# Kernel tuning notes

Hardware: AMD Instinct MI355X
Metric: run time of the kernel (lower is better)

The kernel has to match this reference:

```python
import jax, jax.numpy as jnp
import numpy as np

HEADS = 16

def setup_inputs() -> dict:
    key = jax.random.key(0)
    ks = jax.random.split(key, 5)
    dim = 1024
    x = jax.random.normal(ks[0], (2, 2048, dim), dtype=jnp.float32)
    scale = 1.0 / np.sqrt(dim)
    Wq = jax.random.normal(ks[1], (dim, dim), dtype=jnp.float32) * scale
    Wk = jax.random.normal(ks[2], (dim, dim), dtype=jnp.float32) * scale
    Wv = jax.random.normal(ks[3], (dim, dim), dtype=jnp.float32) * scale
    Wo = jax.random.normal(ks[4], (dim, dim), dtype=jnp.float32) * scale
    return {"x": x, "Wq": Wq, "Wk": Wk, "Wv": Wv, "Wo": Wo}

def reference(x, Wq, Wk, Wv, Wo):
    b, n, dim = x.shape
    h = HEADS
    d = dim // h
    # projections: torch Linear y = x @ W.T (W is [out,in])
    def split_heads(t):
        return t.reshape(b, n, h, d).transpose(0, 2, 1, 3)  # b h n d
    q = split_heads(x @ Wq.T)
    k = split_heads(x @ Wk.T)
    v = split_heads(x @ Wv.T)
    scale = jnp.asarray(d, x.dtype) ** -0.5
    dots = jnp.einsum('bhid,bhjd->bhij', q, k) * scale
    # causal mask: positions j > i masked (triu with diagonal 1 since i == j)
    i_idx = jnp.arange(n)[:, None]
    j_idx = jnp.arange(n)[None, :]
    mask_value = -jnp.finfo(dots.dtype).max
    dots = jnp.where(j_idx > i_idx, mask_value, dots)
    attn = jax.nn.softmax(dots, axis=-1)  # dropout p=0 (eval) is identity
    out = jnp.einsum('bhij,bhjd->bhid', attn, v)
    out = out.transpose(0, 2, 1, 3).reshape(b, n, dim)
    return out @ Wo.T
```

## Files before the change

### kernel.cpp

```cpp
#include <hip/hip_runtime.h>
#include <hip/hip_bf16.h>

#define BATCH 2
#define SEQ   2048
#define DIM   1024
#define HEADS 16
#define DIMH  64
#define BK    32
#define LOG2E 1.44269504088896340736f
#define SM_SHIFT 16.0f

typedef __attribute__((ext_vector_type(8))) short short8;
typedef __attribute__((ext_vector_type(4))) short short4v;
typedef __attribute__((ext_vector_type(4))) float floatx4;

static __device__ __forceinline__ void gload_lds16(const void* g, void* l) {
    __builtin_amdgcn_global_load_lds(
        (const __attribute__((address_space(1))) void*)g,
        (__attribute__((address_space(3))) void*)l, 16, 0, 0);
}

static __device__ __forceinline__ unsigned pk_trunc(float a, float b) {
    return (__float_as_uint(b) & 0xffff0000u) | (__float_as_uint(a) >> 16);
}

__global__ __launch_bounds__(256) void conv_all(
    const float* __restrict__ x,  const float* __restrict__ Wq,
    const float* __restrict__ Wk, const float* __restrict__ Wv,
    const float* __restrict__ Wo,
    __hip_bfloat16* __restrict__ dst, __hip_bfloat16* __restrict__ dwo)
{
    const size_t NX = (size_t)BATCH * SEQ * DIM;
    const size_t NW = (size_t)DIM * DIM;
    size_t i = ((size_t)blockIdx.x * 256 + threadIdx.x) * 4;
    if (i >= NX + 4 * NW) return;
    const float* src; __hip_bfloat16* d;
    if (i < NX) { src = x + i; d = dst + i; }
    else if (i < NX + 3 * NW) {
        size_t j = i - NX;
        int w = (int)(j >> 20);
        src = ((w == 0) ? Wq : (w == 1) ? Wk : Wv) + (j & (NW - 1));
        d = dst + i;
    } else {
        size_t off = i - (NX + 3 * NW);
        src = Wo + off; d = dwo + off;
    }
    floatx4 f = *reinterpret_cast<const floatx4*>(src);
    short4v o;
    #pragma unroll
    for (int e = 0; e < 4; ++e) {
        __hip_bfloat16 t = __float2bfloat16(f[e]);
        o[e] = *reinterpret_cast<short*>(&t);
    }
    *reinterpret_cast<short4v*>(d) = o;
}

__global__ __launch_bounds__(256) void gemm_qkv(
    const __hip_bfloat16* __restrict__ xbf,
    const __hip_bfloat16* __restrict__ wbf,
    __hip_bfloat16* __restrict__ qkv)
{
    __shared__ __align__(16) short As[128 * BK];
    __shared__ __align__(16) short Bs[128 * BK];

    const int tid  = threadIdx.x;
    const int wv   = tid >> 6;
    const int lane = tid & 63;
    const int quad = lane >> 4;
    const int l16  = lane & 15;
    const int wm   = wv >> 1, wn = wv & 1;
    const int m0   = blockIdx.x * 128;
    const int n0   = blockIdx.y * 128;
    const int z    = n0 >> 10;
    __hip_bfloat16* out = qkv + (size_t)z * (BATCH * SEQ * DIM);

    const int srow = tid >> 2;
    const int scol = (tid & 3) * 8;

    floatx4 acc[4][4] = {};

    for (int k0 = 0; k0 < DIM; k0 += BK) {
        __syncthreads();
        #pragma unroll
        for (int i = 0; i < 2; ++i) {
            const __hip_bfloat16* ga = xbf + (size_t)(m0 + srow + i * 64) * DIM + k0 + scol;
            const __hip_bfloat16* gb = wbf + (size_t)(n0 + srow + i * 64) * DIM + k0 + scol;
            gload_lds16(ga, (char*)As + i * 4096 + wv * 1024);
            gload_lds16(gb, (char*)Bs + i * 4096 + wv * 1024);
        }
        __syncthreads();

        short8 af[4], bf[4];
        #pragma unroll
        for (int mt = 0; mt < 4; ++mt)
            af[mt] = *reinterpret_cast<const short8*>(&As[(wm * 64 + mt * 16 + l16) * 32 + quad * 8]);
        #pragma unroll
        for (int nt = 0; nt < 4; ++nt)
            bf[nt] = *reinterpret_cast<const short8*>(&Bs[(wn * 64 + nt * 16 + l16) * 32 + quad * 8]);
        #pragma unroll
        for (int mt = 0; mt < 4; ++mt)
            #pragma unroll
            for (int nt = 0; nt < 4; ++nt)
                acc[mt][nt] = __builtin_amdgcn_mfma_f32_16x16x32_bf16(
                    af[mt], bf[nt], acc[mt][nt], 0, 0, 0);
    }

    const float esc = (z == 0) ? (0.125f * LOG2E) : 1.0f;
    #pragma unroll
    for (int mt = 0; mt < 4; ++mt) {
        #pragma unroll
        for (int nt = 0; nt < 4; ++nt) {
            const int n  = n0 + wn * 64 + nt * 16 + l16;
            const int hh = (n >> 6) & 15, dv = n & 63;
            #pragma unroll
            for (int r = 0; r < 4; ++r) {
                const int m  = m0 + wm * 64 + mt * 16 + quad * 4 + r;
                const int bb = m >> 11, nn = m & (SEQ - 1);
                const float v = acc[mt][nt][r] * esc;
                if (z < 2)
                    out[((size_t)(bb * HEADS + hh) * SEQ + nn) * DIMH + dv] = __float2bfloat16(v);
                else
                    out[((size_t)(bb * HEADS + hh) * DIMH + dv) * SEQ + nn] = __float2bfloat16(v);
            }
        }
    }
}

__global__ __launch_bounds__(256) void gemm_out(
    const __hip_bfloat16* __restrict__ qhs,
    const __hip_bfloat16* __restrict__ W,
    float* __restrict__ C)
{
    __shared__ __align__(16) short As[128 * BK];
    __shared__ __align__(16) short Bs[128 * BK];

    const int tid  = threadIdx.x;
    const int wv   = tid >> 6;
    const int lane = tid & 63;
    const int quad = lane >> 4;
    const int l16  = lane & 15;
    const int wm   = wv >> 1, wn = wv & 1;
    const int m0   = blockIdx.x * 128;
    const int n0   = blockIdx.y * 128;

    const int srow = tid >> 2;
    const int scol = (tid & 3) * 8;

    floatx4 acc[4][4] = {};

    for (int k0 = 0; k0 < DIM; k0 += BK) {
        const int h    = k0 >> 6;
        const int koff = k0 & 63;
        __syncthreads();
        #pragma unroll
        for (int i = 0; i < 2; ++i) {
            const int m  = m0 + srow + i * 64;
            const int bb = m >> 11, nn = m & (SEQ - 1);
            gload_lds16(qhs + ((size_t)(bb * HEADS + h) * SEQ + nn) * DIMH + koff + scol,
                        (char*)As + i * 4096 + wv * 1024);
            gload_lds16(W + (size_t)(n0 + srow + i * 64) * DIM + k0 + scol,
                        (char*)Bs + i * 4096 + wv * 1024);
        }
        __syncthreads();

        short8 af[4], bf[4];
        #pragma unroll
        for (int mt = 0; mt < 4; ++mt)
            af[mt] = *reinterpret_cast<const short8*>(&As[(wm * 64 + mt * 16 + l16) * 32 + quad * 8]);
        #pragma unroll
        for (int nt = 0; nt < 4; ++nt)
            bf[nt] = *reinterpret_cast<const short8*>(&Bs[(wn * 64 + nt * 16 + l16) * 32 + quad * 8]);
        #pragma unroll
        for (int mt = 0; mt < 4; ++mt)
            #pragma unroll
            for (int nt = 0; nt < 4; ++nt)
                acc[mt][nt] = __builtin_amdgcn_mfma_f32_16x16x32_bf16(
                    af[mt], bf[nt], acc[mt][nt], 0, 0, 0);
    }

    #pragma unroll
    for (int mt = 0; mt < 4; ++mt)
        #pragma unroll
        for (int nt = 0; nt < 4; ++nt) {
            const int n = n0 + wn * 64 + nt * 16 + l16;
            #pragma unroll
            for (int r = 0; r < 4; ++r) {
                const int m = m0 + wm * 64 + mt * 16 + quad * 4 + r;
                C[(size_t)m * DIM + n] = acc[mt][nt][r];
            }
        }
}

__global__ __launch_bounds__(256) void attn_causal(
    __hip_bfloat16* __restrict__ qkv)
{
    __shared__ __align__(16) short kt[64 * 64];
    __shared__ __align__(16) short vt[64 * 64];
    __shared__ __align__(16) short pt[2][16 * 72];

    const int id    = blockIdx.x;
    const int combo = id & 31;
    const int p     = id >> 5;
    const int b     = combo >> 4;
    const int h     = combo & 15;
    const int tA = p, tB = 63 - p;
    const int nA = (tA + 2) >> 1;
    const int nB = (tB + 2) >> 1;
    const int total = nA + nB;

    const size_t hoff = (size_t)(b * HEADS + h) * SEQ * DIMH;
    const size_t one  = (size_t)BATCH * SEQ * DIM;
    __hip_bfloat16* qb        = qkv + hoff;
    const __hip_bfloat16* kb  = qkv + one + hoff;
    const __hip_bfloat16* vtg = qkv + 2 * one + hoff;

    const int tid  = threadIdx.x;
    const int wv   = tid >> 6;
    const int g    = wv >> 1;
    const int jh   = wv & 1;
    const int lane = tid & 63;
    const int quad = lane >> 4;
    const int l16  = lane & 15;
    const int xr   = l16 & 7;

    const short8 kone8 = {0x3F80, 0x3F80, 0x3F80, 0x3F80,
                          0x3F80, 0x3F80, 0x3F80, 0x3F80};

    int q16 = tA * 32 + g * 16;
    short8 aq0 = *reinterpret_cast<const short8*>(qb + (size_t)(q16 + l16) * DIMH + quad * 8);
    short8 aq1 = *reinterpret_cast<const short8*>(qb + (size_t)(q16 + l16) * DIMH + 32 + quad * 8);
    floatx4 oacc[4] = {};
    floatx4 lsum = {};

    short8 kreg[2], vreg[2];
    #pragma unroll
    for (int i = 0; i < 2; ++i) {
        const int c = tid + 256 * i;
        const int row = c >> 3, jc = c & 7;
        kreg[i] = *reinterpret_cast<const short8*>(kb + (size_t)row * DIMH + jc * 8);
        vreg[i] = *reinterpret_cast<const short8*>(vtg + (size_t)row * SEQ + jc * 8);
    }

    for (int s = 0; s < total; ++s) {
        const bool lastA = (s == nA - 1);
        const int j0 = ((s < nA) ? s : s - nA) * 64;

        __syncthreads();
        #pragma unroll
        for (int i = 0; i < 2; ++i) {
            const int c = tid + 256 * i;
            const int row = c >> 3, jc = c & 7;
            const int off = row * 64 + ((jc ^ (row & 7)) * 8);
            *reinterpret_cast<short8*>(&kt[off]) = kreg[i];
            *reinterpret_cast<short8*>(&vt[off]) = vreg[i];
        }
        __syncthreads();

        if (s + 1 < total) {
            const int s2 = s + 1;
            const int j1 = ((s2 < nA) ? s2 : s2 - nA) * 64;
            #pragma unroll
            for (int i = 0; i < 2; ++i) {
                const int c = tid + 256 * i;
                const int row = c >> 3, jc = c & 7;
                kreg[i] = *reinterpret_cast<const short8*>(kb + (size_t)(j1 + row) * DIMH + jc * 8);
                vreg[i] = *reinterpret_cast<const short8*>(vtg + (size_t)row * SEQ + j1 + jc * 8);
            }
        }

        floatx4 st[2];
        #pragma unroll
        for (int tt = 0; tt < 2; ++tt) {
            const int t  = jh * 2 + tt;
            const int rw = t * 16 + l16;
            short8 a0 = *reinterpret_cast<const short8*>(&kt[rw * 64 + (quad ^ xr) * 8]);
            short8 a1 = *reinterpret_cast<const short8*>(&kt[rw * 64 + ((quad + 4) ^ xr) * 8]);
            floatx4 zz = {};
            zz     = __builtin_amdgcn_mfma_f32_16x16x32_bf16(a0, aq0, zz, 0, 0, 0);
            st[tt] = __builtin_amdgcn_mfma_f32_16x16x32_bf16(a1, aq1, zz, 0, 0, 0);
        }

        if (j0 + 63 > q16) {
            const int qg = q16 + l16;
            #pragma unroll
            for (int tt = 0; tt < 2; ++tt)
                #pragma unroll
                for (int r = 0; r < 4; ++r) {
                    const int jg = j0 + (jh * 2 + tt) * 16 + quad * 4 + r;
                    if (jg > qg) st[tt][r] = -3.0e38f;
                }
        }

        #pragma unroll
        for (int tt = 0; tt < 2; ++tt)
            #pragma unroll
            for (int r = 0; r < 4; ++r)
                st[tt][r] = __builtin_amdgcn_exp2f(st[tt][r] - SM_SHIFT);

        #pragma unroll
        for (int tt = 0; tt < 2; ++tt) {
            const int t = jh * 2 + tt;
            *reinterpret_cast<unsigned*>(&pt[g][l16 * 72 + t * 16 + quad * 4]) =
                pk_trunc(st[tt][0], st[tt][1]);
            *reinterpret_cast<unsigned*>(&pt[g][l16 * 72 + t * 16 + quad * 4 + 2]) =
                pk_trunc(st[tt][2], st[tt][3]);
        }
        short8 ph = *reinterpret_cast<const short8*>(&pt[g][l16 * 72 + jh * 32 + quad * 8]);

        lsum = __builtin_amdgcn_mfma_f32_16x16x32_bf16(kone8, ph, lsum, 0, 0, 0);

        #pragma unroll
        for (int dt = 0; dt < 4; ++dt) {
            const int rw = dt * 16 + l16;
            short8 vh = *reinterpret_cast<const short8*>(&vt[rw * 64 + ((quad + 4 * jh) ^ xr) * 8]);
            oacc[dt] = __builtin_amdgcn_mfma_f32_16x16x32_bf16(vh, ph, oacc[dt], 0, 0, 0);
        }

        if (lastA || s == total - 1) {
            __syncthreads();
            float* xch = reinterpret_cast<float*>(kt);
            float* xls = reinterpret_cast<float*>(vt);
            if (jh == 1) {
                #pragma unroll
                for (int dt = 0; dt < 4; ++dt)
                    #pragma unroll
                    for (int r = 0; r < 4; ++r)
                        xch[g * 1024 + (dt * 4 + r) * 64 + lane] = oacc[dt][r];
                xls[g * 64 + lane] = lsum[0];
            }
            __syncthreads();
            if (jh == 0) {
                const float rl = 1.0f / (lsum[0] + xls[g * 64 + lane]);
                #pragma unroll
                for (int dt = 0; dt < 4; ++dt)
                    #pragma unroll
                    for (int r = 0; r < 4; ++r) {
                        const float ov = oacc[dt][r] + xch[g * 1024 + (dt * 4 + r) * 64 + lane];
                        qb[(size_t)(q16 + l16) * DIMH + dt * 16 + quad * 4 + r] =
                            __float2bfloat16(ov * rl);
                    }
            }
            if (lastA) {
                q16 = tB * 32 + g * 16;
                aq0 = *reinterpret_cast<const short8*>(qb + (size_t)(q16 + l16) * DIMH + quad * 8);
                aq1 = *reinterpret_cast<const short8*>(qb + (size_t)(q16 + l16) * DIMH + 32 + quad * 8);
                #pragma unroll
                for (int dt = 0; dt < 4; ++dt)
                    #pragma unroll
                    for (int r = 0; r < 4; ++r) oacc[dt][r] = 0.f;
                #pragma unroll
                for (int r = 0; r < 4; ++r) lsum[r] = 0.f;
            }
        }
    }
}


extern "C" void kernel_launch(void* const* d_in, const int* in_sizes, int n_in,
                              void* d_out, int out_size, void* d_ws, size_t ws_size,
                              hipStream_t stream) {
    const float* x  = (const float*)d_in[0];
    const float* Wq = (const float*)d_in[1];
    const float* Wk = (const float*)d_in[2];
    const float* Wv = (const float*)d_in[3];
    const float* Wo = (const float*)d_in[4];

    __hip_bfloat16* qkv  = (__hip_bfloat16*)d_ws;
    __hip_bfloat16* wobf = (__hip_bfloat16*)((char*)d_ws + (size_t)24 * 1024 * 1024);

    __hip_bfloat16* xbf = (__hip_bfloat16*)d_out;
    __hip_bfloat16* wbf = xbf + (size_t)BATCH * SEQ * DIM;

    conv_all  <<<8192, 256, 0, stream>>>(x, Wq, Wk, Wv, Wo, xbf, wobf);
    gemm_qkv  <<<dim3((BATCH * SEQ) / 128, (3 * DIM) / 128), 256, 0, stream>>>(xbf, wbf, qkv);
    attn_causal<<<dim3(1024), 256, 0, stream>>>(qkv);
    gemm_out  <<<dim3((BATCH * SEQ) / 128, DIM / 128), 256, 0, stream>>>(qkv, wobf, (float*)d_out);
}
```

Before: 189.0 us.

## Process two K/V tiles per barrier pair in causal attention

The attention loop now stages two 64-row K/V tiles per iteration into doubled LDS buffers, so each pair of tiles shares one pair of block barriers instead of paying a barrier pair per tile. Register prefetch covers two tiles ahead, and the A/B segments run as separate loops with the output epilogue between them. This cuts synchronisation cost and gives more independent MFMA work between barriers, at the price of twice the LDS and more prefetch registers, which may lower occupancy.

```diff
diff --git a/kernel.cpp b/kernel.cpp
--- a/kernel.cpp
+++ b/kernel.cpp
@@ -194,8 +194,8 @@
 __global__ __launch_bounds__(256) void attn_causal(
     __hip_bfloat16* __restrict__ qkv)
 {
-    __shared__ __align__(16) short kt[64 * 64];
-    __shared__ __align__(16) short vt[64 * 64];
+    __shared__ __align__(16) short kt[2][64 * 64];
+    __shared__ __align__(16) short vt[2][64 * 64];
     __shared__ __align__(16) short pt[2][16 * 72];
 
     const int id    = blockIdx.x;
@@ -206,7 +206,6 @@
     const int tA = p, tB = 63 - p;
     const int nA = (tA + 2) >> 1;
     const int nB = (tB + 2) >> 1;
-    const int total = nA + nB;
 
     const size_t hoff = (size_t)(b * HEADS + h) * SEQ * DIMH;
     const size_t one  = (size_t)BATCH * SEQ * DIM;
@@ -232,127 +231,143 @@
     floatx4 oacc[4] = {};
     floatx4 lsum = {};
 
-    short8 kreg[2], vreg[2];
-    #pragma unroll
-    for (int i = 0; i < 2; ++i) {
-        const int c = tid + 256 * i;
-        const int row = c >> 3, jc = c & 7;
-        kreg[i] = *reinterpret_cast<const short8*>(kb + (size_t)row * DIMH + jc * 8);
-        vreg[i] = *reinterpret_cast<const short8*>(vtg + (size_t)row * SEQ + jc * 8);
-    }
-
-    for (int s = 0; s < total; ++s) {
-        const bool lastA = (s == nA - 1);
-        const int j0 = ((s < nA) ? s : s - nA) * 64;
-
-        __syncthreads();
-        #pragma unroll
-        for (int i = 0; i < 2; ++i) {
-            const int c = tid + 256 * i;
-            const int row = c >> 3, jc = c & 7;
-            const int off = row * 64 + ((jc ^ (row & 7)) * 8);
-            *reinterpret_cast<short8*>(&kt[off]) = kreg[i];
-            *reinterpret_cast<short8*>(&vt[off]) = vreg[i];
-        }
-        __syncthreads();
-
-        if (s + 1 < total) {
-            const int s2 = s + 1;
-            const int j1 = ((s2 < nA) ? s2 : s2 - nA) * 64;
-            #pragma unroll
-            for (int i = 0; i < 2; ++i) {
-                const int c = tid + 256 * i;
-                const int row = c >> 3, jc = c & 7;
-                kreg[i] = *reinterpret_cast<const short8*>(kb + (size_t)(j1 + row) * DIMH + jc * 8);
-                vreg[i] = *reinterpret_cast<const short8*>(vtg + (size_t)row * SEQ + j1 + jc * 8);
+    short8 kreg[4], vreg[4];
+
+#define LOADREG(slot, j0v) do {                                                     \
+    _Pragma("unroll")                                                               \
+    for (int i_ = 0; i_ < 2; ++i_) {                                                \
+        const int cc_ = tid + 256 * i_;                                             \
+        const int row_ = cc_ >> 3, jc_ = cc_ & 7;                                   \
+        kreg[(slot) * 2 + i_] = *reinterpret_cast<const short8*>(                   \
+            kb + (size_t)((j0v) + row_) * DIMH + jc_ * 8);                          \
+        vreg[(slot) * 2 + i_] = *reinterpret_cast<const short8*>(                   \
+            vtg + (size_t)row_ * SEQ + (j0v) + jc_ * 8);                            \
+    } } while (0)
+
+#define COMMIT(slot) do {                                                           \
+    _Pragma("unroll")                                                               \
+    for (int i_ = 0; i_ < 2; ++i_) {                                                \
+        const int cc_ = tid + 256 * i_;                                             \
+        const int row_ = cc_ >> 3, jc_ = cc_ & 7;                                   \
+        const int off_ = row_ * 64 + ((jc_ ^ (row_ & 7)) * 8);                      \
+        *reinterpret_cast<short8*>(&kt[slot][off_]) = kreg[(slot) * 2 + i_];        \
+        *reinterpret_cast<short8*>(&vt[slot][off_]) = vreg[(slot) * 2 + i_];        \
+    } } while (0)
+
+#define COMPUTE(slot, j0v) do {                                                     \
+    const int j0_ = (j0v);                                                          \
+    floatx4 st_[2];                                                                 \
+    _Pragma("unroll")                                                               \
+    for (int tt_ = 0; tt_ < 2; ++tt_) {                                             \
+        const int t_  = jh * 2 + tt_;                                               \
+        const int rw_ = t_ * 16 + l16;                                              \
+        short8 a0_ = *reinterpret_cast<const short8*>(                              \
+            &kt[slot][rw_ * 64 + (quad ^ xr) * 8]);                                 \
+        short8 a1_ = *reinterpret_cast<const short8*>(                              \
+            &kt[slot][rw_ * 64 + ((quad + 4) ^ xr) * 8]);                           \
+        floatx4 zz_ = {};                                                           \
+        zz_     = __builtin_amdgcn_mfma_f32_16x16x32_bf16(a0_, aq0, zz_, 0, 0, 0);  \
+        st_[tt_] = __builtin_amdgcn_mfma_f32_16x16x32_bf16(a1_, aq1, zz_, 0, 0, 0); \
+    }                                                                               \
+    if (j0_ + 63 > q16) {                                                           \
+        const int qg_ = q16 + l16;                                                  \
+        _Pragma("unroll")                                                           \
+        for (int tt_ = 0; tt_ < 2; ++tt_)                                           \
+            _Pragma("unroll")                                                       \
+            for (int r_ = 0; r_ < 4; ++r_) {                                        \
+                const int jg_ = j0_ + (jh * 2 + tt_) * 16 + quad * 4 + r_;          \
+                if (jg_ > qg_) st_[tt_][r_] = -3.0e38f;                             \
+            }                                                                       \
+    }                                                                               \
+    _Pragma("unroll")                                                               \
+    for (int tt_ = 0; tt_ < 2; ++tt_)                                               \
+        _Pragma("unroll")                                                           \
+        for (int r_ = 0; r_ < 4; ++r_)                                              \
+            st_[tt_][r_] = __builtin_amdgcn_exp2f(st_[tt_][r_] - SM_SHIFT);         \
+    _Pragma("unroll")                                                               \
+    for (int tt_ = 0; tt_ < 2; ++tt_) {                                             \
+        const int t_ = jh * 2 + tt_;                                                \
+        *reinterpret_cast<unsigned*>(&pt[g][l16 * 72 + t_ * 16 + quad * 4]) =       \
+            pk_trunc(st_[tt_][0], st_[tt_][1]);                                     \
+        *reinterpret_cast<unsigned*>(&pt[g][l16 * 72 + t_ * 16 + quad * 4 + 2]) =   \
+            pk_trunc(st_[tt_][2], st_[tt_][3]);                                     \
+    }                                                                               \
+    short8 ph_ = *reinterpret_cast<const short8*>(                                  \
+        &pt[g][l16 * 72 + jh * 32 + quad * 8]);                                     \
+    lsum = __builtin_amdgcn_mfma_f32_16x16x32_bf16(kone8, ph_, lsum, 0, 0, 0);      \
+    _Pragma("unroll")                                                               \
+    for (int dt_ = 0; dt_ < 4; ++dt_) {                                             \
+        const int rw_ = dt_ * 16 + l16;                                             \
+        short8 vh_ = *reinterpret_cast<const short8*>(                              \
+            &vt[slot][rw_ * 64 + ((quad + 4 * jh) ^ xr) * 8]);                      \
+        oacc[dt_] = __builtin_amdgcn_mfma_f32_16x16x32_bf16(vh_, ph_, oacc[dt_], 0, 0, 0); \
+    } } while (0)
+
+    LOADREG(0, 0);
+    if (nA >= 2) LOADREG(1, 64);
+
+    for (int seg = 0; seg < 2; ++seg) {
+        const int n = seg ? nB : nA;
+        for (int s = 0; s < n; s += 2) {
+            const int cnt = (n - s >= 2) ? 2 : 1;
+
+            __syncthreads();
+            COMMIT(0);
+            if (cnt == 2) COMMIT(1);
+            __syncthreads();
+
+            int ns = s + 2, nseg = seg;
+            if (ns >= n) { ns = 0; nseg = seg + 1; }
+            if (nseg < 2) {
+                const int nn2  = nseg ? nB : nA;
+                const int ncnt = (nn2 - ns >= 2) ? 2 : 1;
+                LOADREG(0, ns * 64);
+                if (ncnt == 2) LOADREG(1, ns * 64 + 64);
             }
-        }
-
-        floatx4 st[2];
-        #pragma unroll
-        for (int tt = 0; tt < 2; ++tt) {
-            const int t  = jh * 2 + tt;
-            const int rw = t * 16 + l16;
-            short8 a0 = *reinterpret_cast<const short8*>(&kt[rw * 64 + (quad ^ xr) * 8]);
-            short8 a1 = *reinterpret_cast<const short8*>(&kt[rw * 64 + ((quad + 4) ^ xr) * 8]);
-            floatx4 zz = {};
-            zz     = __builtin_amdgcn_mfma_f32_16x16x32_bf16(a0, aq0, zz, 0, 0, 0);
-            st[tt] = __builtin_amdgcn_mfma_f32_16x16x32_bf16(a1, aq1, zz, 0, 0, 0);
-        }
-
-        if (j0 + 63 > q16) {
-            const int qg = q16 + l16;
-            #pragma unroll
-            for (int tt = 0; tt < 2; ++tt)
+
+            COMPUTE(0, s * 64);
+            if (cnt == 2) COMPUTE(1, s * 64 + 64);
+        }
+
+        __syncthreads();
+        float* xch = reinterpret_cast<float*>(kt);
+        float* xls = reinterpret_cast<float*>(vt);
+        if (jh == 1) {
+            #pragma unroll
+            for (int dt = 0; dt < 4; ++dt)
+                #pragma unroll
+                for (int r = 0; r < 4; ++r)
+                    xch[g * 1024 + (dt * 4 + r) * 64 + lane] = oacc[dt][r];
+            xls[g * 64 + lane] = lsum[0];
+        }
+        __syncthreads();
+        if (jh == 0) {
+            const float rl = 1.0f / (lsum[0] + xls[g * 64 + lane]);
+            #pragma unroll
+            for (int dt = 0; dt < 4; ++dt)
                 #pragma unroll
                 for (int r = 0; r < 4; ++r) {
-                    const int jg = j0 + (jh * 2 + tt) * 16 + quad * 4 + r;
-                    if (jg > qg) st[tt][r] = -3.0e38f;
+                    const float ov = oacc[dt][r] + xch[g * 1024 + (dt * 4 + r) * 64 + lane];
+                    qb[(size_t)(q16 + l16) * DIMH + dt * 16 + quad * 4 + r] =
+                        __float2bfloat16(ov * rl);
                 }
         }
-
-        #pragma unroll
-        for (int tt = 0; tt < 2; ++tt)
-            #pragma unroll
-            for (int r = 0; r < 4; ++r)
-                st[tt][r] = __builtin_amdgcn_exp2f(st[tt][r] - SM_SHIFT);
-
-        #pragma unroll
-        for (int tt = 0; tt < 2; ++tt) {
-            const int t = jh * 2 + tt;
-            *reinterpret_cast<unsigned*>(&pt[g][l16 * 72 + t * 16 + quad * 4]) =
-                pk_trunc(st[tt][0], st[tt][1]);
-            *reinterpret_cast<unsigned*>(&pt[g][l16 * 72 + t * 16 + quad * 4 + 2]) =
-                pk_trunc(st[tt][2], st[tt][3]);
-        }
-        short8 ph = *reinterpret_cast<const short8*>(&pt[g][l16 * 72 + jh * 32 + quad * 8]);
-
-        lsum = __builtin_amdgcn_mfma_f32_16x16x32_bf16(kone8, ph, lsum, 0, 0, 0);
-
-        #pragma unroll
-        for (int dt = 0; dt < 4; ++dt) {
-            const int rw = dt * 16 + l16;
-            short8 vh = *reinterpret_cast<const short8*>(&vt[rw * 64 + ((quad + 4 * jh) ^ xr) * 8]);
-            oacc[dt] = __builtin_amdgcn_mfma_f32_16x16x32_bf16(vh, ph, oacc[dt], 0, 0, 0);
-        }
-
-        if (lastA || s == total - 1) {
-            __syncthreads();
-            float* xch = reinterpret_cast<float*>(kt);
-            float* xls = reinterpret_cast<float*>(vt);
-            if (jh == 1) {
+        if (seg == 0) {
+            q16 = tB * 32 + g * 16;
+            aq0 = *reinterpret_cast<const short8*>(qb + (size_t)(q16 + l16) * DIMH + quad * 8);
+            aq1 = *reinterpret_cast<const short8*>(qb + (size_t)(q16 + l16) * DIMH + 32 + quad * 8);
+            #pragma unroll
+            for (int dt = 0; dt < 4; ++dt)
                 #pragma unroll
-                for (int dt = 0; dt < 4; ++dt)
-                    #pragma unroll
-                    for (int r = 0; r < 4; ++r)
-                        xch[g * 1024 + (dt * 4 + r) * 64 + lane] = oacc[dt][r];
-                xls[g * 64 + lane] = lsum[0];
-            }
-            __syncthreads();
-            if (jh == 0) {
-                const float rl = 1.0f / (lsum[0] + xls[g * 64 + lane]);
-                #pragma unroll
-                for (int dt = 0; dt < 4; ++dt)
-                    #pragma unroll
-                    for (int r = 0; r < 4; ++r) {
-                        const float ov = oacc[dt][r] + xch[g * 1024 + (dt * 4 + r) * 64 + lane];
-                        qb[(size_t)(q16 + l16) * DIMH + dt * 16 + quad * 4 + r] =
-                            __float2bfloat16(ov * rl);
-                    }
-            }
-            if (lastA) {
-                q16 = tB * 32 + g * 16;
-                aq0 = *reinterpret_cast<const short8*>(qb + (size_t)(q16 + l16) * DIMH + quad * 8);
-                aq1 = *reinterpret_cast<const short8*>(qb + (size_t)(q16 + l16) * DIMH + 32 + quad * 8);
-                #pragma unroll
-                for (int dt = 0; dt < 4; ++dt)
-                    #pragma unroll
-                    for (int r = 0; r < 4; ++r) oacc[dt][r] = 0.f;
-                #pragma unroll
-                for (int r = 0; r < 4; ++r) lsum[r] = 0.f;
-            }
-        }
-    }
+                for (int r = 0; r < 4; ++r) oacc[dt][r] = 0.f;
+            #pragma unroll
+            for (int r = 0; r < 4; ++r) lsum[r] = 0.f;
+        }
+    }
+
+#undef LOADREG
+#undef COMMIT
+#undef COMPUTE
 }
 
 
```

Result: no change. 189.5 us (+0.3%).

## Load K and V fragments directly from global into registers, drop LDS staging

Applied to the files above, without the earlier changes.

The attention kernel no longer stages K and V tiles through shared memory with two block-wide barriers per step. Each wave now loads its MFMA operand fragments for K and V straight from global memory, double-buffering K in registers and loading V each iteration. This removes the per-step LDS writes, reads and __syncthreads. In exchange, the two waves sharing a query group each fetch their own slices with less coalesced 16-byte accesses, and the V loads are not prefetched, so their latency may be exposed.

```diff
diff --git a/kernel.cpp b/kernel.cpp
--- a/kernel.cpp
+++ b/kernel.cpp
@@ -194,9 +194,9 @@
 __global__ __launch_bounds__(256) void attn_causal(
     __hip_bfloat16* __restrict__ qkv)
 {
-    __shared__ __align__(16) short kt[64 * 64];
-    __shared__ __align__(16) short vt[64 * 64];
     __shared__ __align__(16) short pt[2][16 * 72];
+    __shared__ __align__(16) float xch[2][1024];
+    __shared__ float xls[2][64];
 
     const int id    = blockIdx.x;
     const int combo = id & 31;
@@ -221,7 +221,6 @@
     const int lane = tid & 63;
     const int quad = lane >> 4;
     const int l16  = lane & 15;
-    const int xr   = l16 & 7;
 
     const short8 kone8 = {0x3F80, 0x3F80, 0x3F80, 0x3F80,
                           0x3F80, 0x3F80, 0x3F80, 0x3F80};
@@ -232,52 +231,44 @@
     floatx4 oacc[4] = {};
     floatx4 lsum = {};
 
-    short8 kreg[2], vreg[2];
+    const size_t kbase = (size_t)(jh * 32 + l16) * DIMH + quad * 8;
+    const size_t vbase = (size_t)l16 * SEQ + jh * 32 + quad * 8;
+
+    short8 kc[2][2], kn[2][2];
     #pragma unroll
-    for (int i = 0; i < 2; ++i) {
-        const int c = tid + 256 * i;
-        const int row = c >> 3, jc = c & 7;
-        kreg[i] = *reinterpret_cast<const short8*>(kb + (size_t)row * DIMH + jc * 8);
-        vreg[i] = *reinterpret_cast<const short8*>(vtg + (size_t)row * SEQ + jc * 8);
-    }
+    for (int tt = 0; tt < 2; ++tt)
+        #pragma unroll
+        for (int hf = 0; hf < 2; ++hf)
+            kc[tt][hf] = *reinterpret_cast<const short8*>(
+                kb + kbase + (size_t)tt * 16 * DIMH + hf * 32);
 
     for (int s = 0; s < total; ++s) {
         const bool lastA = (s == nA - 1);
         const int j0 = ((s < nA) ? s : s - nA) * 64;
 
-        __syncthreads();
-        #pragma unroll
-        for (int i = 0; i < 2; ++i) {
-            const int c = tid + 256 * i;
-            const int row = c >> 3, jc = c & 7;
-            const int off = row * 64 + ((jc ^ (row & 7)) * 8);
-            *reinterpret_cast<short8*>(&kt[off]) = kreg[i];
-            *reinterpret_cast<short8*>(&vt[off]) = vreg[i];
-        }
-        __syncthreads();
+        short8 vc[4];
+        #pragma unroll
+        for (int dt = 0; dt < 4; ++dt)
+            vc[dt] = *reinterpret_cast<const short8*>(
+                vtg + vbase + (size_t)dt * 16 * SEQ + j0);
+
+        floatx4 st[2];
+        #pragma unroll
+        for (int tt = 0; tt < 2; ++tt) {
+            floatx4 zz = {};
+            zz     = __builtin_amdgcn_mfma_f32_16x16x32_bf16(kc[tt][0], aq0, zz, 0, 0, 0);
+            st[tt] = __builtin_amdgcn_mfma_f32_16x16x32_bf16(kc[tt][1], aq1, zz, 0, 0, 0);
+        }
 
         if (s + 1 < total) {
             const int s2 = s + 1;
             const int j1 = ((s2 < nA) ? s2 : s2 - nA) * 64;
             #pragma unroll
-            for (int i = 0; i < 2; ++i) {
-                const int c = tid + 256 * i;
-                const int row = c >> 3, jc = c & 7;
-                kreg[i] = *reinterpret_cast<const short8*>(kb + (size_t)(j1 + row) * DIMH + jc * 8);
-                vreg[i] = *reinterpret_cast<const short8*>(vtg + (size_t)row * SEQ + j1 + jc * 8);
-            }
-        }
-
-        floatx4 st[2];
-        #pragma unroll
-        for (int tt = 0; tt < 2; ++tt) {
-            const int t  = jh * 2 + tt;
-            const int rw = t * 16 + l16;
-            short8 a0 = *reinterpret_cast<const short8*>(&kt[rw * 64 + (quad ^ xr) * 8]);
-            short8 a1 = *reinterpret_cast<const short8*>(&kt[rw * 64 + ((quad + 4) ^ xr) * 8]);
-            floatx4 zz = {};
-            zz     = __builtin_amdgcn_mfma_f32_16x16x32_bf16(a0, aq0, zz, 0, 0, 0);
-            st[tt] = __builtin_amdgcn_mfma_f32_16x16x32_bf16(a1, aq1, zz, 0, 0, 0);
+            for (int tt = 0; tt < 2; ++tt)
+                #pragma unroll
+                for (int hf = 0; hf < 2; ++hf)
+                    kn[tt][hf] = *reinterpret_cast<const short8*>(
+                        kb + kbase + (size_t)(j1 + tt * 16) * DIMH + hf * 32);
         }
 
         if (j0 + 63 > q16) {
@@ -310,32 +301,27 @@
         lsum = __builtin_amdgcn_mfma_f32_16x16x32_bf16(kone8, ph, lsum, 0, 0, 0);
 
         #pragma unroll
-        for (int dt = 0; dt < 4; ++dt) {
-            const int rw = dt * 16 + l16;
-            short8 vh = *reinterpret_cast<const short8*>(&vt[rw * 64 + ((quad + 4 * jh) ^ xr) * 8]);
-            oacc[dt] = __builtin_amdgcn_mfma_f32_16x16x32_bf16(vh, ph, oacc[dt], 0, 0, 0);
-        }
+        for (int dt = 0; dt < 4; ++dt)
+            oacc[dt] = __builtin_amdgcn_mfma_f32_16x16x32_bf16(vc[dt], ph, oacc[dt], 0, 0, 0);
 
         if (lastA || s == total - 1) {
             __syncthreads();
-            float* xch = reinterpret_cast<float*>(kt);
-            float* xls = reinterpret_cast<float*>(vt);
             if (jh == 1) {
                 #pragma unroll
                 for (int dt = 0; dt < 4; ++dt)
                     #pragma unroll
                     for (int r = 0; r < 4; ++r)
-                        xch[g * 1024 + (dt * 4 + r) * 64 + lane] = oacc[dt][r];
-                xls[g * 64 + lane] = lsum[0];
+                        xch[g][(dt * 4 + r) * 64 + lane] = oacc[dt][r];
+                xls[g][lane] = lsum[0];
             }
             __syncthreads();
             if (jh == 0) {
-                const float rl = 1.0f / (lsum[0] + xls[g * 64 + lane]);
+                const float rl = 1.0f / (lsum[0] + xls[g][lane]);
                 #pragma unroll
                 for (int dt = 0; dt < 4; ++dt)
                     #pragma unroll
                     for (int r = 0; r < 4; ++r) {
-                        const float ov = oacc[dt][r] + xch[g * 1024 + (dt * 4 + r) * 64 + lane];
+                        const float ov = oacc[dt][r] + xch[g][(dt * 4 + r) * 64 + lane];
                         qb[(size_t)(q16 + l16) * DIMH + dt * 16 + quad * 4 + r] =
                             __float2bfloat16(ov * rl);
                     }
@@ -352,6 +338,12 @@
                 for (int r = 0; r < 4; ++r) lsum[r] = 0.f;
             }
         }
+
+        #pragma unroll
+        for (int tt = 0; tt < 2; ++tt)
+            #pragma unroll
+            for (int hf = 0; hf < 2; ++hf)
+                kc[tt][hf] = kn[tt][hf];
     }
 }
 
```

After: 262.3 us. 1.39x slower.

## Double GEMM K-tile to 64 with XOR-swizzled LDS and raise MFMA wave priority

Applied to the files above, without the earlier changes.

Both projection GEMMs now stage a 64-wide K slice per iteration instead of 32. Each LDS row chunk is XOR-swizzled so the wider rows avoid bank conflicts on the MFMA fragment reads. This halves the number of barrier pairs and load phases per GEMM, at the cost of double the shared memory per block, which can lower occupancy. In the attention kernel, s_setprio brackets the MFMA sections so waves issuing matrix ops get scheduling priority over waves doing softmax work.

```diff
diff --git a/kernel.cpp b/kernel.cpp
--- a/kernel.cpp
+++ b/kernel.cpp
@@ -6,7 +6,7 @@
 #define DIM   1024
 #define HEADS 16
 #define DIMH  64
-#define BK    32
+#define BK    64
 #define LOG2E 1.44269504088896340736f
 #define SM_SHIFT 16.0f
 
@@ -74,35 +74,41 @@
     const int z    = n0 >> 10;
     __hip_bfloat16* out = qkv + (size_t)z * (BATCH * SEQ * DIM);
 
-    const int srow = tid >> 2;
-    const int scol = (tid & 3) * 8;
+    const int srow = tid >> 3;
+    const int scol = ((tid & 7) ^ (srow & 7)) * 8;
+    const int xr   = l16 & 7;
 
     floatx4 acc[4][4] = {};
 
     for (int k0 = 0; k0 < DIM; k0 += BK) {
         __syncthreads();
         #pragma unroll
-        for (int i = 0; i < 2; ++i) {
-            const __hip_bfloat16* ga = xbf + (size_t)(m0 + srow + i * 64) * DIM + k0 + scol;
-            const __hip_bfloat16* gb = wbf + (size_t)(n0 + srow + i * 64) * DIM + k0 + scol;
+        for (int i = 0; i < 4; ++i) {
+            const __hip_bfloat16* ga = xbf + (size_t)(m0 + i * 32 + srow) * DIM + k0 + scol;
+            const __hip_bfloat16* gb = wbf + (size_t)(n0 + i * 32 + srow) * DIM + k0 + scol;
             gload_lds16(ga, (char*)As + i * 4096 + wv * 1024);
             gload_lds16(gb, (char*)Bs + i * 4096 + wv * 1024);
         }
         __syncthreads();
 
-        short8 af[4], bf[4];
-        #pragma unroll
-        for (int mt = 0; mt < 4; ++mt)
-            af[mt] = *reinterpret_cast<const short8*>(&As[(wm * 64 + mt * 16 + l16) * 32 + quad * 8]);
-        #pragma unroll
-        for (int nt = 0; nt < 4; ++nt)
-            bf[nt] = *reinterpret_cast<const short8*>(&Bs[(wn * 64 + nt * 16 + l16) * 32 + quad * 8]);
-        #pragma unroll
-        for (int mt = 0; mt < 4; ++mt)
+        #pragma unroll
+        for (int kk = 0; kk < 2; ++kk) {
+            short8 af[4], bf[4];
+            #pragma unroll
+            for (int mt = 0; mt < 4; ++mt)
+                af[mt] = *reinterpret_cast<const short8*>(
+                    &As[(wm * 64 + mt * 16 + l16) * 64 + (((kk * 4 + quad) ^ xr) * 8)]);
             #pragma unroll
             for (int nt = 0; nt < 4; ++nt)
-                acc[mt][nt] = __builtin_amdgcn_mfma_f32_16x16x32_bf16(
-                    af[mt], bf[nt], acc[mt][nt], 0, 0, 0);
+                bf[nt] = *reinterpret_cast<const short8*>(
+                    &Bs[(wn * 64 + nt * 16 + l16) * 64 + (((kk * 4 + quad) ^ xr) * 8)]);
+            #pragma unroll
+            for (int mt = 0; mt < 4; ++mt)
+                #pragma unroll
+                for (int nt = 0; nt < 4; ++nt)
+                    acc[mt][nt] = __builtin_amdgcn_mfma_f32_16x16x32_bf16(
+                        af[mt], bf[nt], acc[mt][nt], 0, 0, 0);
+        }
     }
 
     const float esc = (z == 0) ? (0.125f * LOG2E) : 1.0f;
@@ -143,39 +149,44 @@
     const int m0   = blockIdx.x * 128;
     const int n0   = blockIdx.y * 128;
 
-    const int srow = tid >> 2;
-    const int scol = (tid & 3) * 8;
+    const int srow = tid >> 3;
+    const int scol = ((tid & 7) ^ (srow & 7)) * 8;
+    const int xr   = l16 & 7;
 
     floatx4 acc[4][4] = {};
 
     for (int k0 = 0; k0 < DIM; k0 += BK) {
-        const int h    = k0 >> 6;
-        const int koff = k0 & 63;
-        __syncthreads();
-        #pragma unroll
-        for (int i = 0; i < 2; ++i) {
-            const int m  = m0 + srow + i * 64;
+        const int h = k0 >> 6;
+        __syncthreads();
+        #pragma unroll
+        for (int i = 0; i < 4; ++i) {
+            const int m  = m0 + i * 32 + srow;
             const int bb = m >> 11, nn = m & (SEQ - 1);
-            gload_lds16(qhs + ((size_t)(bb * HEADS + h) * SEQ + nn) * DIMH + koff + scol,
+            gload_lds16(qhs + ((size_t)(bb * HEADS + h) * SEQ + nn) * DIMH + scol,
                         (char*)As + i * 4096 + wv * 1024);
-            gload_lds16(W + (size_t)(n0 + srow + i * 64) * DIM + k0 + scol,
+            gload_lds16(W + (size_t)(n0 + i * 32 + srow) * DIM + k0 + scol,
                         (char*)Bs + i * 4096 + wv * 1024);
         }
         __syncthreads();
 
-        short8 af[4], bf[4];
-        #pragma unroll
-        for (int mt = 0; mt < 4; ++mt)
-            af[mt] = *reinterpret_cast<const short8*>(&As[(wm * 64 + mt * 16 + l16) * 32 + quad * 8]);
-        #pragma unroll
-        for (int nt = 0; nt < 4; ++nt)
-            bf[nt] = *reinterpret_cast<const short8*>(&Bs[(wn * 64 + nt * 16 + l16) * 32 + quad * 8]);
-        #pragma unroll
-        for (int mt = 0; mt < 4; ++mt)
+        #pragma unroll
+        for (int kk = 0; kk < 2; ++kk) {
+            short8 af[4], bf[4];
+            #pragma unroll
+            for (int mt = 0; mt < 4; ++mt)
+                af[mt] = *reinterpret_cast<const short8*>(
+                    &As[(wm * 64 + mt * 16 + l16) * 64 + (((kk * 4 + quad) ^ xr) * 8)]);
             #pragma unroll
             for (int nt = 0; nt < 4; ++nt)
-                acc[mt][nt] = __builtin_amdgcn_mfma_f32_16x16x32_bf16(
-                    af[mt], bf[nt], acc[mt][nt], 0, 0, 0);
+                bf[nt] = *reinterpret_cast<const short8*>(
+                    &Bs[(wn * 64 + nt * 16 + l16) * 64 + (((kk * 4 + quad) ^ xr) * 8)]);
+            #pragma unroll
+            for (int mt = 0; mt < 4; ++mt)
+                #pragma unroll
+                for (int nt = 0; nt < 4; ++nt)
+                    acc[mt][nt] = __builtin_amdgcn_mfma_f32_16x16x32_bf16(
+                        af[mt], bf[nt], acc[mt][nt], 0, 0, 0);
+        }
     }
 
     #pragma unroll
@@ -269,6 +280,7 @@
         }
 
         floatx4 st[2];
+        __builtin_amdgcn_s_setprio(1);
         #pragma unroll
         for (int tt = 0; tt < 2; ++tt) {
             const int t  = jh * 2 + tt;
@@ -279,6 +291,7 @@
             zz     = __builtin_amdgcn_mfma_f32_16x16x32_bf16(a0, aq0, zz, 0, 0, 0);
             st[tt] = __builtin_amdgcn_mfma_f32_16x16x32_bf16(a1, aq1, zz, 0, 0, 0);
         }
+        __builtin_amdgcn_s_setprio(0);
 
         if (j0 + 63 > q16) {
             const int qg = q16 + l16;
@@ -307,14 +320,17 @@
         }
         short8 ph = *reinterpret_cast<const short8*>(&pt[g][l16 * 72 + jh * 32 + quad * 8]);
 
+        __builtin_amdgcn_s_setprio(1);
         lsum = __builtin_amdgcn_mfma_f32_16x16x32_bf16(kone8, ph, lsum, 0, 0, 0);
 
         #pragma unroll
         for (int dt = 0; dt < 4; ++dt) {
             const int rw = dt * 16 + l16;
-            short8 vh = *reinterpret_cast<const short8*>(&vt[rw * 64 + ((quad + 4 * jh) ^ xr) * 8]);
+            short8 vh = *reinterpret_cast<const short8*>(
+                &vt[rw * 64 + ((quad + 4 * jh) ^ xr) * 8]);
             oacc[dt] = __builtin_amdgcn_mfma_f32_16x16x32_bf16(vh, ph, oacc[dt], 0, 0, 0);
         }
+        __builtin_amdgcn_s_setprio(0);
 
         if (lastA || s == total - 1) {
             __syncthreads();
```

Result: slower. 194.9 us (+3.1%).
